# Kernel tuning notes

Hardware: AMD Instinct MI355X
Metric: run time of the kernel (lower is better)

## Reference

```python
import jax, jax.numpy as jnp
import numpy as np

B, S, D, H = 2, 2048, 1024, 16
DK = D // H


def setup_inputs() -> dict:
    key = jax.random.key(0)
    ks = jax.random.split(key, 11)
    s_in = 1.0 / np.sqrt(D)
    return {
        "query": jax.random.normal(ks[0], (B, S, D), jnp.float32),
        "key_": jax.random.normal(ks[1], (B, S, D), jnp.float32),
        "value": jax.random.normal(ks[2], (B, S, D), jnp.float32),
        "W_q": jax.random.normal(ks[3], (D, D), jnp.float32) * s_in,
        "b_q": jnp.zeros((D,), jnp.float32),
        "W_k": jax.random.normal(ks[4], (D, D), jnp.float32) * s_in,
        "b_k": jnp.zeros((D,), jnp.float32),
        "W_v": jax.random.normal(ks[5], (D, D), jnp.float32) * s_in,
        "b_v": jnp.zeros((D,), jnp.float32),
        "W_o": jax.random.normal(ks[6], (D, D), jnp.float32) * s_in,
        "b_o": jnp.zeros((D,), jnp.float32),
    }


def _split_heads(x):
    # [B,S,D] -> [B,H,S,DK]
    b, s, _ = x.shape
    return x.reshape(b, s, H, DK).transpose(0, 2, 1, 3)


def reference(query, key_, value, W_q, b_q, W_k, b_k, W_v, b_v, W_o, b_o):
    q = _split_heads(query @ W_q.T + b_q)
    k = _split_heads(key_ @ W_k.T + b_k)
    v = _split_heads(value @ W_v.T + b_v)
    scores = jnp.einsum("bhqd,bhkd->bhqk", q, k) / jnp.sqrt(jnp.float32(DK))
    attention_weights = jax.nn.softmax(scores, axis=-1)  # [B,H,S,S]
    # dropout is identity in eval mode
    context = jnp.einsum("bhqk,bhkd->bhqd", attention_weights, v)
    context = context.transpose(0, 2, 1, 3).reshape(query.shape[0], -1, D)
    output = context @ W_o.T + b_o
    return (output, attention_weights)
```

## Files before the change

kernel.cpp:

```cpp
#include <hip/hip_runtime.h>
#include <hip/hip_bf16.h>

#define B_DIM 2
#define S_DIM 2048
#define D_DIM 1024
#define H_DIM 16
#define DK_DIM 64

typedef __attribute__((ext_vector_type(8))) short short8;
typedef __attribute__((ext_vector_type(4))) float floatx4;

__device__ __forceinline__ unsigned short f2bf(float f) {
    unsigned u = __builtin_bit_cast(unsigned, f);
    u += 0x7fff + ((u >> 16) & 1);
    return (unsigned short)(u >> 16);
}

#define GLDS16(g, l) __builtin_amdgcn_global_load_lds( \
    (const __attribute__((address_space(1))) void*)(g), \
    (__attribute__((address_space(3))) void*)(l), 16, 0, 0)

template <int ROWS>
__device__ __forceinline__ void stage_tile(const unsigned short* __restrict__ src, int ld,
                                           short* lds, int tid) {
#pragma unroll
    for (int r = 0; r < ROWS / 32; ++r) {
        int t = r * 256 + tid;
        const unsigned short* g = src + (size_t)(t >> 3) * ld + ((t & 7) << 3);
        short* dst = lds + ((size_t)(r * 256 + (tid >> 6) * 64) << 3);
        GLDS16(g, dst);
    }
}

template <int ROWS>
__device__ __forceinline__ void stage_cvt(const float* __restrict__ src, int ld,
                                          short* lds, int tid) {
#pragma unroll
    for (int i = 0; i < ROWS / 16; ++i) {
        int f = i * 256 + tid;
        int row = f >> 4, c4 = (f & 15) << 2;
        float4 v = *(const float4*)(src + (size_t)row * ld + c4);
        union { ushort4 u; uint2 d; } p;
        p.u.x = f2bf(v.x); p.u.y = f2bf(v.y); p.u.z = f2bf(v.z); p.u.w = f2bf(v.w);
        *(uint2*)&lds[row * 64 + c4] = p.d;
    }
}

struct GemmBatchF {
    const float* A[3];
    const float* W[3];
    const float* bias[3];
    void* C[3];
    int mode[3];
};

__global__ __launch_bounds__(256) void gemm_f32bt(GemmBatchF p, int N, int K) {
    __shared__ short At[128 * 64];
    __shared__ short Bt[128 * 64];
    int z = blockIdx.z;
    const float* A = p.A[z];
    const float* W = p.W[z];
    const float* bias = p.bias[z];
    void* Cv = p.C[z];
    int mode = p.mode[z];

    int tid = threadIdx.x;
    int wave = tid >> 6, lane = tid & 63;
    int l15 = lane & 15, quad = lane >> 4;
    int bn = blockIdx.x, bm = blockIdx.y;
    const float* Ab = A + (size_t)bm * 128 * K;
    const float* Wb = W + (size_t)bn * 128 * K;
    int wm = (wave >> 1) * 64, wn = (wave & 1) * 64;

    floatx4 acc[4][4] = {};
    for (int k0 = 0; k0 < K; k0 += 64) {
        __syncthreads();
        stage_cvt<128>(Ab + k0, K, At, tid);
        stage_cvt<128>(Wb + k0, K, Bt, tid);
        __syncthreads();
#pragma unroll
        for (int kk = 0; kk < 2; ++kk) {
            short8 af[4], bf[4];
#pragma unroll
            for (int i = 0; i < 4; ++i)
                af[i] = *(const short8*)&At[(wm + i * 16 + l15) * 64 + kk * 32 + quad * 8];
#pragma unroll
            for (int j = 0; j < 4; ++j)
                bf[j] = *(const short8*)&Bt[(wn + j * 16 + l15) * 64 + kk * 32 + quad * 8];
#pragma unroll
            for (int i = 0; i < 4; ++i)
#pragma unroll
                for (int j = 0; j < 4; ++j)
                    acc[i][j] = __builtin_amdgcn_mfma_f32_16x16x32_bf16(af[i], bf[j], acc[i][j], 0, 0, 0);
        }
    }

    int row0 = bm * 128 + wm + quad * 4;
    int col0 = bn * 128 + wn + l15;
    if (mode == 0) {
        unsigned short* C = (unsigned short*)Cv;
#pragma unroll
        for (int j = 0; j < 4; ++j) {
            int col = col0 + j * 16;
            float bc = bias[col];
#pragma unroll
            for (int i = 0; i < 4; ++i) {
                int row = row0 + i * 16;
#pragma unroll
                for (int r = 0; r < 4; ++r)
                    C[(size_t)(row + r) * N + col] = f2bf(acc[i][j][r] + bc);
            }
        }
    } else if (mode == 1) {
        unsigned short* C = (unsigned short*)Cv;
#pragma unroll
        for (int j = 0; j < 4; ++j) {
            int col = col0 + j * 16;
            float bc = bias[col];
            int h = col >> 6, dk = col & 63;
#pragma unroll
            for (int i = 0; i < 4; ++i) {
                int row = row0 + i * 16;
                int b = row >> 11, s = row & 2047;
                size_t base = (((size_t)(b * 16 + h) * 64 + dk) << 11) + s;
                uint2 pk;
                pk.x = (unsigned)f2bf(acc[i][j][0] + bc) | ((unsigned)f2bf(acc[i][j][1] + bc) << 16);
                pk.y = (unsigned)f2bf(acc[i][j][2] + bc) | ((unsigned)f2bf(acc[i][j][3] + bc) << 16);
                *(uint2*)(C + base) = pk;
            }
        }
    } else {
        float* C = (float*)Cv;
#pragma unroll
        for (int j = 0; j < 4; ++j) {
            int col = col0 + j * 16;
            float bc = bias[col];
#pragma unroll
            for (int i = 0; i < 4; ++i) {
                int row = row0 + i * 16;
#pragma unroll
                for (int r = 0; r < 4; ++r)
                    C[(size_t)(row + r) * N + col] = acc[i][j][r] + bc;
            }
        }
    }
}

__global__ __launch_bounds__(256) void attn_scores(const unsigned short* __restrict__ q_ws,
                                                   const unsigned short* __restrict__ k_ws,
                                                   float* __restrict__ wout) {
    __shared__ short Qt[64 * 64];
    __shared__ short Kt[64 * 64];
    int tid = threadIdx.x;
    int wave = tid >> 6, lane = tid & 63;
    int l15 = lane & 15, quad = lane >> 4;
    int bh = blockIdx.y;
    int b = bh >> 4, h = bh & 15;
    int q0 = blockIdx.x * 64;
    const unsigned short* Qb = q_ws + (size_t)b * S_DIM * D_DIM + h * 64;
    const unsigned short* Kb = k_ws + (size_t)b * S_DIM * D_DIM + h * 64;

    stage_tile<64>(Qb + (size_t)q0 * D_DIM, D_DIM, Qt, tid);
    __syncthreads();
    short8 a0 = *(const short8*)&Qt[(wave * 16 + l15) * 64 + quad * 8];
    short8 a1 = *(const short8*)&Qt[(wave * 16 + l15) * 64 + 32 + quad * 8];

    const float SC = 0.18033688011112042f;
    float m[4], l[4];
#pragma unroll
    for (int r = 0; r < 4; ++r) { m[r] = -__builtin_inff(); l[r] = 0.f; }

    for (int kt = 0; kt < 32; ++kt) {
        __syncthreads();
        stage_tile<64>(Kb + (size_t)kt * 64 * D_DIM, D_DIM, Kt, tid);
        __syncthreads();
        floatx4 acc[4] = {};
#pragma unroll
        for (int j = 0; j < 4; ++j) {
            short8 b0 = *(const short8*)&Kt[(j * 16 + l15) * 64 + quad * 8];
            short8 b1 = *(const short8*)&Kt[(j * 16 + l15) * 64 + 32 + quad * 8];
            acc[j] = __builtin_amdgcn_mfma_f32_16x16x32_bf16(a0, b0, acc[j], 0, 0, 0);
            acc[j] = __builtin_amdgcn_mfma_f32_16x16x32_bf16(a1, b1, acc[j], 0, 0, 0);
        }
        float v[4][4];
#pragma unroll
        for (int j = 0; j < 4; ++j)
#pragma unroll
            for (int r = 0; r < 4; ++r) v[j][r] = acc[j][r] * SC;
        float tmax[4];
#pragma unroll
        for (int r = 0; r < 4; ++r)
            tmax[r] = fmaxf(fmaxf(v[0][r], v[1][r]), fmaxf(v[2][r], v[3][r]));
#pragma unroll
        for (int off = 1; off < 16; off <<= 1)
#pragma unroll
            for (int r = 0; r < 4; ++r)
                tmax[r] = fmaxf(tmax[r], __shfl_xor(tmax[r], off));
        float alpha[4], ps[4];
#pragma unroll
        for (int r = 0; r < 4; ++r) {
            float mn = fmaxf(m[r], tmax[r]);
            alpha[r] = exp2f(m[r] - mn);
            m[r] = mn;
            ps[r] = exp2f(v[0][r] - mn) + exp2f(v[1][r] - mn) +
                    exp2f(v[2][r] - mn) + exp2f(v[3][r] - mn);
        }
#pragma unroll
        for (int off = 1; off < 16; off <<= 1)
#pragma unroll
            for (int r = 0; r < 4; ++r)
                ps[r] += __shfl_xor(ps[r], off);
#pragma unroll
        for (int r = 0; r < 4; ++r) l[r] = l[r] * alpha[r] + ps[r];
    }
    float rl[4];
#pragma unroll
    for (int r = 0; r < 4; ++r) rl[r] = 1.0f / l[r];

    float* wrow = wout + ((size_t)bh * S_DIM + q0 + wave * 16 + quad * 4) * (size_t)S_DIM;
    for (int kt = 0; kt < 32; ++kt) {
        __syncthreads();
        stage_tile<64>(Kb + (size_t)kt * 64 * D_DIM, D_DIM, Kt, tid);
        __syncthreads();
        floatx4 acc[4] = {};
#pragma unroll
        for (int j = 0; j < 4; ++j) {
            short8 b0 = *(const short8*)&Kt[(j * 16 + l15) * 64 + quad * 8];
            short8 b1 = *(const short8*)&Kt[(j * 16 + l15) * 64 + 32 + quad * 8];
            acc[j] = __builtin_amdgcn_mfma_f32_16x16x32_bf16(a0, b0, acc[j], 0, 0, 0);
            acc[j] = __builtin_amdgcn_mfma_f32_16x16x32_bf16(a1, b1, acc[j], 0, 0, 0);
        }
#pragma unroll
        for (int j = 0; j < 4; ++j) {
            int colo = kt * 64 + j * 16 + l15;
#pragma unroll
            for (int r = 0; r < 4; ++r) {
                float w = exp2f(acc[j][r] * SC - m[r]) * rl[r];
                wrow[(size_t)r * S_DIM + colo] = w;
            }
        }
    }
}

__global__ __launch_bounds__(256) void pv_gemm(const float* __restrict__ P,
                                               const unsigned short* __restrict__ vT,
                                               float* __restrict__ ctx) {
    __shared__ short Pt[128 * 64];
    __shared__ short Vt[64 * 64];
    int tid = threadIdx.x;
    int wave = tid >> 6, lane = tid & 63;
    int l15 = lane & 15, quad = lane >> 4;
    int bh = blockIdx.y;
    int b = bh >> 4, h = bh & 15;
    int m0 = blockIdx.x * 128;
    const float* Pb = P + (size_t)bh * S_DIM * S_DIM + (size_t)m0 * S_DIM;
    const unsigned short* Vb = vT + (size_t)bh * 64 * S_DIM;
    int wm = wave * 32;

    floatx4 acc[2][4] = {};
    for (int k0 = 0; k0 < S_DIM; k0 += 64) {
        __syncthreads();
        stage_cvt<128>(Pb + k0, S_DIM, Pt, tid);
        stage_tile<64>(Vb + k0, S_DIM, Vt, tid);
        __syncthreads();
#pragma unroll
        for (int kk = 0; kk < 2; ++kk) {
            short8 af[2], bf[4];
#pragma unroll
            for (int i = 0; i < 2; ++i)
                af[i] = *(const short8*)&Pt[(wm + i * 16 + l15) * 64 + kk * 32 + quad * 8];
#pragma unroll
            for (int j = 0; j < 4; ++j)
                bf[j] = *(const short8*)&Vt[(j * 16 + l15) * 64 + kk * 32 + quad * 8];
#pragma unroll
            for (int i = 0; i < 2; ++i)
#pragma unroll
                for (int j = 0; j < 4; ++j)
                    acc[i][j] = __builtin_amdgcn_mfma_f32_16x16x32_bf16(af[i], bf[j], acc[i][j], 0, 0, 0);
        }
    }
    int row0 = m0 + wm + quad * 4;
#pragma unroll
    for (int i = 0; i < 2; ++i)
#pragma unroll
        for (int j = 0; j < 4; ++j) {
            int dk = j * 16 + l15;
#pragma unroll
            for (int r = 0; r < 4; ++r) {
                int s = row0 + i * 16 + r;
                ctx[((size_t)b * S_DIM + s) * D_DIM + h * 64 + dk] = acc[i][j][r];
            }
        }
}

extern "C" void kernel_launch(void* const* d_in, const int* in_sizes, int n_in,
                              void* d_out, int out_size, void* d_ws, size_t ws_size,
                              hipStream_t stream) {
    const float* query = (const float*)d_in[0];
    const float* key_  = (const float*)d_in[1];
    const float* value = (const float*)d_in[2];
    const float* W_q = (const float*)d_in[3];
    const float* b_q = (const float*)d_in[4];
    const float* W_k = (const float*)d_in[5];
    const float* b_k = (const float*)d_in[6];
    const float* W_v = (const float*)d_in[7];
    const float* b_v = (const float*)d_in[8];
    const float* W_o = (const float*)d_in[9];
    const float* b_o = (const float*)d_in[10];

    float* out  = (float*)d_out;
    float* wout = out + (size_t)4096 * 1024;

    unsigned short* q_ws = (unsigned short*)d_ws;
    unsigned short* k_ws = q_ws + (size_t)4096 * 1024;
    unsigned short* vT   = k_ws + (size_t)4096 * 1024;
    float* ctx = (float*)d_ws;

    GemmBatchF p1;
    p1.A[0] = query; p1.A[1] = key_; p1.A[2] = value;
    p1.W[0] = W_q;   p1.W[1] = W_k;  p1.W[2] = W_v;
    p1.bias[0] = b_q; p1.bias[1] = b_k; p1.bias[2] = b_v;
    p1.C[0] = q_ws;  p1.C[1] = k_ws; p1.C[2] = vT;
    p1.mode[0] = 0;  p1.mode[1] = 0; p1.mode[2] = 1;
    gemm_f32bt<<<dim3(8, 32, 3), 256, 0, stream>>>(p1, 1024, 1024);

    attn_scores<<<dim3(32, 32), 256, 0, stream>>>(q_ws, k_ws, wout);

    pv_gemm<<<dim3(16, 32), 256, 0, stream>>>(wout, vT, ctx);

    GemmBatchF p4;
    for (int i = 0; i < 3; ++i) {
        p4.A[i] = ctx; p4.W[i] = W_o; p4.bias[i] = b_o; p4.C[i] = out; p4.mode[i] = 2;
    }
    gemm_f32bt<<<dim3(8, 32, 1), 256, 0, stream>>>(p4, 1024, 1024);
}
```

Baseline: 1.303 ms.

## Fuse P·V into attention scores kernel and pass context as bf16

Merges the separate P·V GEMM into the attention kernel's second pass. Each wave converts its normalized probabilities to bf16 in a swizzled LDS tile and immediately runs MFMAs against V, so the huge fp32 attention matrix no longer has to be read back from global memory. K and Q fragments are now loaded directly from global memory instead of through LDS staging, which removes the block-wide barriers but relies on L2 for reuse and gives less coalesced access. The context is written as bf16 into the Q workspace, which is safe because each block only overwrites its own Q slice after reading it. The output projection GEMM gains a bf16-input path so it can consume that context directly.

```diff
diff --git a/kernel.cpp b/kernel.cpp
--- a/kernel.cpp
+++ b/kernel.cpp
@@ -52,6 +52,7 @@
     const float* bias[3];
     void* C[3];
     int mode[3];
+    int abf16[3];
 };
 
 __global__ __launch_bounds__(256) void gemm_f32bt(GemmBatchF p, int N, int K) {
@@ -63,19 +64,22 @@
     const float* bias = p.bias[z];
     void* Cv = p.C[z];
     int mode = p.mode[z];
+    int abf = p.abf16[z];
 
     int tid = threadIdx.x;
     int wave = tid >> 6, lane = tid & 63;
     int l15 = lane & 15, quad = lane >> 4;
     int bn = blockIdx.x, bm = blockIdx.y;
     const float* Ab = A + (size_t)bm * 128 * K;
+    const unsigned short* Abh = (const unsigned short*)A + (size_t)bm * 128 * K;
     const float* Wb = W + (size_t)bn * 128 * K;
     int wm = (wave >> 1) * 64, wn = (wave & 1) * 64;
 
     floatx4 acc[4][4] = {};
     for (int k0 = 0; k0 < K; k0 += 64) {
         __syncthreads();
-        stage_cvt<128>(Ab + k0, K, At, tid);
+        if (abf) stage_tile<128>(Abh + k0, K, At, tid);
+        else     stage_cvt<128>(Ab + k0, K, At, tid);
         stage_cvt<128>(Wb + k0, K, Bt, tid);
         __syncthreads();
 #pragma unroll
@@ -146,24 +150,30 @@
     }
 }
 
-__global__ __launch_bounds__(256) void attn_scores(const unsigned short* __restrict__ q_ws,
-                                                   const unsigned short* __restrict__ k_ws,
-                                                   float* __restrict__ wout) {
-    __shared__ short Qt[64 * 64];
-    __shared__ short Kt[64 * 64];
+__device__ __forceinline__ int pswz(int row, int col) {
+    return (row << 6) + ((((col >> 3) ^ row) & 7) << 3) + (col & 7);
+}
+
+__global__ __launch_bounds__(256) void attn_fused(const unsigned short* q_ws,
+                                                  const unsigned short* __restrict__ k_ws,
+                                                  const unsigned short* __restrict__ vT,
+                                                  float* __restrict__ wout,
+                                                  unsigned short* ctx_bf) {
+    __shared__ short Pt[4 * 16 * 64];
     int tid = threadIdx.x;
     int wave = tid >> 6, lane = tid & 63;
     int l15 = lane & 15, quad = lane >> 4;
     int bh = blockIdx.y;
     int b = bh >> 4, h = bh & 15;
     int q0 = blockIdx.x * 64;
-    const unsigned short* Qb = q_ws + (size_t)b * S_DIM * D_DIM + h * 64;
+
+    const unsigned short* Qp =
+        q_ws + (size_t)(b * S_DIM + q0 + wave * 16 + l15) * D_DIM + h * 64 + quad * 8;
+    short8 a0 = *(const short8*)Qp;
+    short8 a1 = *(const short8*)(Qp + 32);
+
     const unsigned short* Kb = k_ws + (size_t)b * S_DIM * D_DIM + h * 64;
-
-    stage_tile<64>(Qb + (size_t)q0 * D_DIM, D_DIM, Qt, tid);
-    __syncthreads();
-    short8 a0 = *(const short8*)&Qt[(wave * 16 + l15) * 64 + quad * 8];
-    short8 a1 = *(const short8*)&Qt[(wave * 16 + l15) * 64 + 32 + quad * 8];
+    const unsigned short* Vb = vT + (size_t)bh * 64 * S_DIM;
 
     const float SC = 0.18033688011112042f;
     float m[4], l[4];
@@ -171,14 +181,13 @@
     for (int r = 0; r < 4; ++r) { m[r] = -__builtin_inff(); l[r] = 0.f; }
 
     for (int kt = 0; kt < 32; ++kt) {
-        __syncthreads();
-        stage_tile<64>(Kb + (size_t)kt * 64 * D_DIM, D_DIM, Kt, tid);
-        __syncthreads();
+        const unsigned short* Kt = Kb + (size_t)(kt * 64) * D_DIM;
         floatx4 acc[4] = {};
 #pragma unroll
         for (int j = 0; j < 4; ++j) {
-            short8 b0 = *(const short8*)&Kt[(j * 16 + l15) * 64 + quad * 8];
-            short8 b1 = *(const short8*)&Kt[(j * 16 + l15) * 64 + 32 + quad * 8];
+            const unsigned short* kp = Kt + (size_t)(j * 16 + l15) * D_DIM + quad * 8;
+            short8 b0 = *(const short8*)kp;
+            short8 b1 = *(const short8*)(kp + 32);
             acc[j] = __builtin_amdgcn_mfma_f32_16x16x32_bf16(a0, b0, acc[j], 0, 0, 0);
             acc[j] = __builtin_amdgcn_mfma_f32_16x16x32_bf16(a1, b1, acc[j], 0, 0, 0);
         }
@@ -217,16 +226,18 @@
 #pragma unroll
     for (int r = 0; r < 4; ++r) rl[r] = 1.0f / l[r];
 
+    short* Pw = &Pt[wave * 16 * 64];
+    floatx4 cacc[4] = {};
     float* wrow = wout + ((size_t)bh * S_DIM + q0 + wave * 16 + quad * 4) * (size_t)S_DIM;
+
     for (int kt = 0; kt < 32; ++kt) {
-        __syncthreads();
-        stage_tile<64>(Kb + (size_t)kt * 64 * D_DIM, D_DIM, Kt, tid);
-        __syncthreads();
+        const unsigned short* Kt = Kb + (size_t)(kt * 64) * D_DIM;
         floatx4 acc[4] = {};
 #pragma unroll
         for (int j = 0; j < 4; ++j) {
-            short8 b0 = *(const short8*)&Kt[(j * 16 + l15) * 64 + quad * 8];
-            short8 b1 = *(const short8*)&Kt[(j * 16 + l15) * 64 + 32 + quad * 8];
+            const unsigned short* kp = Kt + (size_t)(j * 16 + l15) * D_DIM + quad * 8;
+            short8 b0 = *(const short8*)kp;
+            short8 b1 = *(const short8*)(kp + 32);
             acc[j] = __builtin_amdgcn_mfma_f32_16x16x32_bf16(a0, b0, acc[j], 0, 0, 0);
             acc[j] = __builtin_amdgcn_mfma_f32_16x16x32_bf16(a1, b1, acc[j], 0, 0, 0);
         }
@@ -237,60 +248,30 @@
             for (int r = 0; r < 4; ++r) {
                 float w = exp2f(acc[j][r] * SC - m[r]) * rl[r];
                 wrow[(size_t)r * S_DIM + colo] = w;
-            }
-        }
-    }
-}
-
-__global__ __launch_bounds__(256) void pv_gemm(const float* __restrict__ P,
-                                               const unsigned short* __restrict__ vT,
-                                               float* __restrict__ ctx) {
-    __shared__ short Pt[128 * 64];
-    __shared__ short Vt[64 * 64];
-    int tid = threadIdx.x;
-    int wave = tid >> 6, lane = tid & 63;
-    int l15 = lane & 15, quad = lane >> 4;
-    int bh = blockIdx.y;
-    int b = bh >> 4, h = bh & 15;
-    int m0 = blockIdx.x * 128;
-    const float* Pb = P + (size_t)bh * S_DIM * S_DIM + (size_t)m0 * S_DIM;
-    const unsigned short* Vb = vT + (size_t)bh * 64 * S_DIM;
-    int wm = wave * 32;
-
-    floatx4 acc[2][4] = {};
-    for (int k0 = 0; k0 < S_DIM; k0 += 64) {
-        __syncthreads();
-        stage_cvt<128>(Pb + k0, S_DIM, Pt, tid);
-        stage_tile<64>(Vb + k0, S_DIM, Vt, tid);
-        __syncthreads();
+                Pw[pswz(quad * 4 + r, j * 16 + l15)] = (short)f2bf(w);
+            }
+        }
+        asm volatile("s_waitcnt lgkmcnt(0)" ::: "memory");
+        __builtin_amdgcn_sched_barrier(0);
 #pragma unroll
         for (int kk = 0; kk < 2; ++kk) {
-            short8 af[2], bf[4];
-#pragma unroll
-            for (int i = 0; i < 2; ++i)
-                af[i] = *(const short8*)&Pt[(wm + i * 16 + l15) * 64 + kk * 32 + quad * 8];
-#pragma unroll
-            for (int j = 0; j < 4; ++j)
-                bf[j] = *(const short8*)&Vt[(j * 16 + l15) * 64 + kk * 32 + quad * 8];
-#pragma unroll
-            for (int i = 0; i < 2; ++i)
-#pragma unroll
-                for (int j = 0; j < 4; ++j)
-                    acc[i][j] = __builtin_amdgcn_mfma_f32_16x16x32_bf16(af[i], bf[j], acc[i][j], 0, 0, 0);
-        }
-    }
-    int row0 = m0 + wm + quad * 4;
-#pragma unroll
-    for (int i = 0; i < 2; ++i)
-#pragma unroll
-        for (int j = 0; j < 4; ++j) {
-            int dk = j * 16 + l15;
-#pragma unroll
-            for (int r = 0; r < 4; ++r) {
-                int s = row0 + i * 16 + r;
-                ctx[((size_t)b * S_DIM + s) * D_DIM + h * 64 + dk] = acc[i][j][r];
-            }
-        }
+            short8 ap = *(const short8*)&Pw[pswz(l15, kk * 32 + quad * 8)];
+#pragma unroll
+            for (int j = 0; j < 4; ++j) {
+                short8 bv = *(const short8*)&Vb[(size_t)(j * 16 + l15) * S_DIM +
+                                                kt * 64 + kk * 32 + quad * 8];
+                cacc[j] = __builtin_amdgcn_mfma_f32_16x16x32_bf16(ap, bv, cacc[j], 0, 0, 0);
+            }
+        }
+    }
+
+    unsigned short* cb =
+        ctx_bf + (size_t)(b * S_DIM + q0 + wave * 16 + quad * 4) * D_DIM + h * 64;
+#pragma unroll
+    for (int j = 0; j < 4; ++j)
+#pragma unroll
+        for (int r = 0; r < 4; ++r)
+            cb[(size_t)r * D_DIM + j * 16 + l15] = f2bf(cacc[j][r]);
 }
 
 extern "C" void kernel_launch(void* const* d_in, const int* in_sizes, int n_in,
@@ -314,7 +295,7 @@
     unsigned short* q_ws = (unsigned short*)d_ws;
     unsigned short* k_ws = q_ws + (size_t)4096 * 1024;
     unsigned short* vT   = k_ws + (size_t)4096 * 1024;
-    float* ctx = (float*)d_ws;
+    unsigned short* ctx_bf = q_ws;
 
     GemmBatchF p1;
     p1.A[0] = query; p1.A[1] = key_; p1.A[2] = value;
@@ -322,15 +303,15 @@
     p1.bias[0] = b_q; p1.bias[1] = b_k; p1.bias[2] = b_v;
     p1.C[0] = q_ws;  p1.C[1] = k_ws; p1.C[2] = vT;
     p1.mode[0] = 0;  p1.mode[1] = 0; p1.mode[2] = 1;
+    p1.abf16[0] = 0; p1.abf16[1] = 0; p1.abf16[2] = 0;
     gemm_f32bt<<<dim3(8, 32, 3), 256, 0, stream>>>(p1, 1024, 1024);
 
-    attn_scores<<<dim3(32, 32), 256, 0, stream>>>(q_ws, k_ws, wout);
-
-    pv_gemm<<<dim3(16, 32), 256, 0, stream>>>(wout, vT, ctx);
+    attn_fused<<<dim3(32, 32), 256, 0, stream>>>(q_ws, k_ws, vT, wout, ctx_bf);
 
     GemmBatchF p4;
     for (int i = 0; i < 3; ++i) {
-        p4.A[i] = ctx; p4.W[i] = W_o; p4.bias[i] = b_o; p4.C[i] = out; p4.mode[i] = 2;
+        p4.A[i] = (const float*)ctx_bf; p4.W[i] = W_o; p4.bias[i] = b_o;
+        p4.C[i] = out; p4.mode[i] = 2; p4.abf16[i] = 1;
     }
     gemm_f32bt<<<dim3(8, 32, 1), 256, 0, stream>>>(p4, 1024, 1024);
 }
```

Result: faster. 1.197 ms (-8.1%).
